# Kernel optimization log

Hardware: AMD Instinct MI355X
Metric: run time of the kernel (lower is better)

The kernel has to match this reference:

```python
import jax, jax.numpy as jnp
import numpy as np

B, S, D = 2, 2048, 1024
H, KVH, HD = 16, 1, 64
E, K, HID = 8, 2, 4096
EPS = 1e-5


def rmsnorm(x, scale):
    ms = jnp.mean(x * x, axis=-1, keepdims=True)
    return x * jax.lax.rsqrt(ms + EPS) * scale


def setup_inputs() -> dict:
    key = jax.random.key(0)
    ks = jax.random.split(key, 12)
    s = lambda k, shape, fan: jax.random.normal(k, shape, jnp.float32) * (fan ** -0.5)
    return {
        "x": jax.random.normal(ks[0], (B, S, D), jnp.float32),
        "g_pre_mqa": jnp.ones((D,), jnp.float32),
        "g_post_mqa": jnp.ones((D,), jnp.float32),
        "g_pre_moe": jnp.ones((D,), jnp.float32),
        "g_post_moe": jnp.ones((D,), jnp.float32),
        "Wq": s(ks[1], (D, H * HD), D),
        "Wk": s(ks[2], (D, KVH * HD), D),
        "Wv": s(ks[3], (D, KVH * HD), D),
        "Wo": s(ks[4], (H * HD, D), H * HD),
        "Wg": s(ks[5], (D, E), D),
        "We1": s(ks[6], (E, D, HID), D),
        "We2": s(ks[7], (E, HID, D), HID),
    }


def mqa(x, Wq, Wk, Wv, Wo):
    b, s, _ = x.shape
    q = (x @ Wq).reshape(b, s, H, HD).transpose(0, 2, 1, 3)     # [B,H,S,hd]
    k = (x @ Wk).reshape(b, s, KVH, HD).transpose(0, 2, 1, 3)   # [B,1,S,hd]
    v = (x @ Wv).reshape(b, s, KVH, HD).transpose(0, 2, 1, 3)
    scores = jnp.einsum('bhqd,bhkd->bhqk', q, jnp.broadcast_to(k, (b, H, s, HD))) / np.sqrt(HD)
    probs = jax.nn.softmax(scores, axis=-1)  # note: no causal mask, matching _standard_attention
    out = jnp.einsum('bhqk,bhkd->bhqd', probs, jnp.broadcast_to(v, (b, H, s, HD)))
    out = out.transpose(0, 2, 1, 3).reshape(b, s, H * HD)
    return out @ Wo


def moe(h, Wg, We1, We2):
    logits = h @ Wg                       # [B,S,E]
    probs = jax.nn.softmax(logits, axis=-1)
    topv, topi = jax.lax.top_k(probs, K)  # [B,S,K]
    # scatter top-k probs into full expert vector (non-chosen experts -> 0)
    routing = jnp.sum(jax.nn.one_hot(topi, E, dtype=h.dtype) * topv[..., None], axis=-2)  # [B,S,E]
    mid = jax.nn.gelu(jnp.einsum('bsd,edh->bseh', h, We1))
    eo = jnp.einsum('bseh,ehd->bsed', mid, We2)
    out = jnp.einsum('bse,bsed->bsd', routing, eo)
    return out, probs


def reference(x, g_pre_mqa, g_post_mqa, g_pre_moe, g_post_moe, Wq, Wk, Wv, Wo, Wg, We1, We2):
    # inference path: dropout and router noise disabled (training=False)
    x = x + rmsnorm(mqa(rmsnorm(x, g_pre_mqa), Wq, Wk, Wv, Wo), g_post_mqa)
    moe_out, routing_probs = moe(rmsnorm(x, g_pre_moe), Wg, We1, We2)
    x = x + rmsnorm(moe_out, g_post_moe)
    return x, routing_probs
```

## Files before the change

kernel.cpp:

```cpp
#include <hip/hip_runtime.h>
#include <hip/hip_bf16.h>
#include <math.h>

#define NTOK   4096
#define DMODEL 1024
#define SEQL   2048
#define QKVW   1152
#define NH     16
#define HDIM   64
#define NE     8
#define HIDD   4096
#define EPSV   1e-5f
#define KT     32

#define ASCL   256.f
#define WSCL   4096.f
#define OUTSCL (1.f/1048576.f)

typedef __attribute__((ext_vector_type(8))) short bf16x8;
typedef __attribute__((ext_vector_type(8))) _Float16 f16x8;
typedef __attribute__((ext_vector_type(4))) _Float16 f16x4;
typedef __attribute__((ext_vector_type(4))) float f32x4;

__device__ __forceinline__ short f2b(float x){
  __hip_bfloat16 h = __float2bfloat16(x);
  return *reinterpret_cast<short*>(&h);
}
__device__ __forceinline__ float b2f(short s){
  __hip_bfloat16 h = *reinterpret_cast<__hip_bfloat16*>(&s);
  return __bfloat162float(h);
}
__device__ __forceinline__ void split3(float x, short& a, short& b, short& c){
  a = f2b(x);
  float r1 = x - b2f(a);
  b = f2b(r1);
  float r2 = r1 - b2f(b);
  c = f2b(r2);
}
__device__ __forceinline__ void split2h(float x, _Float16& a, _Float16& b){
  a = (_Float16)x;
  b = (_Float16)(x - (float)a);
}

__global__ __launch_bounds__(256) void transpose_conv_kernel(
    const float* __restrict__ in, short* __restrict__ out,
    int R, int C, long inb, long outb)
{
  __shared__ float tile[32][33];
  in  += (size_t)blockIdx.z * inb;
  out += (size_t)blockIdx.z * outb;
  int c0 = blockIdx.x*32, r0 = blockIdx.y*32;
  int tx = threadIdx.x & 31, ty = threadIdx.x >> 5;
  #pragma unroll
  for (int i=0;i<4;i++)
    tile[ty+i*8][tx] = in[(size_t)(r0+ty+i*8)*C + c0+tx];
  __syncthreads();
  #pragma unroll
  for (int i=0;i<4;i++)
    out[(size_t)(c0+ty+i*8)*R + r0+tx] = f2b(tile[tx][ty+i*8]);
}

__global__ __launch_bounds__(256) void transpose_split2f16_kernel(
    const float* __restrict__ in, _Float16* __restrict__ o1, _Float16* __restrict__ o2,
    int R, int C, int rowOff, int outLD)
{
  __shared__ float tile[32][33];
  int c0 = blockIdx.x*32, r0 = blockIdx.y*32;
  int tx = threadIdx.x & 31, ty = threadIdx.x >> 5;
  #pragma unroll
  for (int i=0;i<4;i++)
    tile[ty+i*8][tx] = in[(size_t)(r0+ty+i*8)*C + c0+tx];
  __syncthreads();
  #pragma unroll
  for (int i=0;i<4;i++){
    float v = tile[tx][ty+i*8] * WSCL;
    _Float16 a,b; split2h(v,a,b);
    size_t idx = (size_t)(c0+ty+i*8+rowOff)*outLD + r0+tx;
    o1[idx]=a; o2[idx]=b;
  }
}

__global__ __launch_bounds__(256) void rms_split2_kernel(
    const float* __restrict__ x, const float* __restrict__ g,
    _Float16* __restrict__ o1, _Float16* __restrict__ o2)
{
  int row = blockIdx.x, tid = threadIdx.x;
  const float4* xr = (const float4*)(x + (size_t)row*DMODEL);
  float4 v = xr[tid];
  float ss = v.x*v.x + v.y*v.y + v.z*v.z + v.w*v.w;
  #pragma unroll
  for (int off=32; off; off>>=1) ss += __shfl_down(ss, off);
  __shared__ float red[4];
  if ((tid&63)==0) red[tid>>6] = ss;
  __syncthreads();
  float rs = rsqrtf((red[0]+red[1]+red[2]+red[3])*(1.f/1024.f) + EPSV) * ASCL;
  float4 gv = ((const float4*)g)[tid];
  float o[4] = {v.x*rs*gv.x, v.y*rs*gv.y, v.z*rs*gv.z, v.w*rs*gv.w};
  f16x4 s1,s2;
  #pragma unroll
  for (int c=0;c<4;c++){ _Float16 a,b; split2h(o[c],a,b); s1[c]=a; s2[c]=b; }
  size_t base = (size_t)row*DMODEL + tid*4;
  *(f16x4*)(o1+base) = s1; *(f16x4*)(o2+base) = s2;
}

__global__ void split3_flat_kernel(const float* __restrict__ in,
    short* __restrict__ o1, short* __restrict__ o2, short* __restrict__ o3, int n4)
{
  int i = blockIdx.x*256 + threadIdx.x;
  if (i >= n4) return;
  float4 v = ((const float4*)in)[i];
  short4 s1,s2,s3;
  split3(v.x, s1.x, s2.x, s3.x);
  split3(v.y, s1.y, s2.y, s3.y);
  split3(v.z, s1.z, s2.z, s3.z);
  split3(v.w, s1.w, s2.w, s3.w);
  ((short4*)o1)[i]=s1; ((short4*)o2)[i]=s2; ((short4*)o3)[i]=s3;
}

__global__ __launch_bounds__(256) void vtrans_split3_kernel(
    const float* __restrict__ qkv,
    short* __restrict__ o1, short* __restrict__ o2, short* __restrict__ o3)
{
  __shared__ float tile[32][33];
  int s0 = blockIdx.x*32, d0 = blockIdx.y*32, b = blockIdx.z;
  int tx = threadIdx.x & 31, ty = threadIdx.x >> 5;
  #pragma unroll
  for (int i=0;i<4;i++)
    tile[ty+i*8][tx] = qkv[(size_t)(b*SEQL + s0+ty+i*8)*QKVW + DMODEL+HDIM + d0+tx];
  __syncthreads();
  #pragma unroll
  for (int i=0;i<4;i++){
    float v = tile[tx][ty+i*8];
    short a,bs,c; split3(v,a,bs,c);
    size_t idx = (size_t)(b*HDIM + d0+ty+i*8)*SEQL + s0+tx;
    o1[idx]=a; o2[idx]=bs; o3[idx]=c;
  }
}

__global__ __launch_bounds__(256) void gemm_f16x2_kernel(
    const _Float16* __restrict__ a1, const _Float16* __restrict__ a2,
    const _Float16* __restrict__ b1, const _Float16* __restrict__ b2,
    float* __restrict__ C, int K, int ldc, float outscale)
{
  __shared__ _Float16 lsA[2][128*40];
  __shared__ _Float16 lsB[2][128*40];
  int m0 = blockIdx.y*128, n0 = blockIdx.x*128;
  int tid = threadIdx.x, wave = tid>>6, lane = tid&63;
  int g = lane>>4, li = lane&15;
  int wm = (wave>>1)*64, wn = (wave&1)*64;
  const _Float16* Ap[2] = {a1,a2};
  const _Float16* Bp[2] = {b1,b2};
  f32x4 acc[4][4] = {};
  for (int k0=0; k0<K; k0+=32){
    #pragma unroll
    for (int p=0;p<2;p++){
      #pragma unroll
      for (int i=0;i<2;i++){
        int c = tid + 256*i;
        int row = c>>2, col = (c&3)*8;
        *(f16x8*)&lsA[p][row*40+col] = *(const f16x8*)(Ap[p] + (size_t)(m0+row)*K + k0+col);
        *(f16x8*)&lsB[p][row*40+col] = *(const f16x8*)(Bp[p] + (size_t)(n0+row)*K + k0+col);
      }
    }
    __syncthreads();
    #pragma unroll
    for (int i=0;i<2;i++){
      f16x8 af[4];
      #pragma unroll
      for (int m=0;m<4;m++) af[m] = *(f16x8*)&lsA[i][(wm+m*16+li)*40 + g*8];
      #pragma unroll
      for (int j=0;j<2-i;j++){
        #pragma unroll
        for (int n=0;n<4;n++){
          f16x8 bfr = *(f16x8*)&lsB[j][(wn+n*16+li)*40 + g*8];
          #pragma unroll
          for (int m=0;m<4;m++)
            acc[m][n] = __builtin_amdgcn_mfma_f32_16x16x32_f16(af[m], bfr, acc[m][n], 0,0,0);
        }
      }
    }
    __syncthreads();
  }
  #pragma unroll
  for (int m=0;m<4;m++){
    int lr0 = wm + m*16 + g*4;
    #pragma unroll
    for (int n=0;n<4;n++){
      int col = n0 + wn + n*16 + li;
      #pragma unroll
      for (int r=0;r<4;r++)
        C[(size_t)(m0+lr0+r)*ldc + col] = acc[m][n][r]*outscale;
    }
  }
}

__global__ __launch_bounds__(256) void attn_bf16x3_kernel(
    const short* __restrict__ q1, const short* __restrict__ q2, const short* __restrict__ q3,
    const short* __restrict__ v1, const short* __restrict__ v2, const short* __restrict__ v3,
    _Float16* __restrict__ o1, _Float16* __restrict__ o2)
{
  __shared__ short Qs[128*200];
  __shared__ short Ks[32*200];
  __shared__ short Vs[64*104];
  int qt = blockIdx.x, h = blockIdx.y, b = blockIdx.z;
  int tid = threadIdx.x, wave = tid>>6, lane = tid&63;
  int g = lane>>4, li = lane&15;
  size_t qbase = (size_t)b*SEQL + qt*128;
  const short* qsrc[3] = {q1,q2,q3};
  const short* vsrc[3] = {v1,v2,v3};
  #pragma unroll
  for (int i=0;i<12;i++){
    int c = tid + 256*i;
    int row = c/24, sub = c - row*24;
    int p = sub>>3, d = (sub&7)*8;
    *(bf16x8*)&Qs[row*200 + p*64 + d] =
        *(const bf16x8*)(qsrc[p] + (qbase+row)*QKVW + h*HDIM + d);
  }
  float m_run[2] = {-1e30f,-1e30f}, l_run[2] = {0.f,0.f};
  f32x4 acc_o[4][2] = {};
  int src1 = (((2*g)&3)<<4) + li;
  int src2 = (((2*g+1)&3)<<4) + li;
  bool hi_half = (g>=2);

  for (int kvt=0; kvt<SEQL/KT; kvt++){
    __syncthreads();
    #pragma unroll
    for (int i=0;i<3;i++){
      int c = tid + 256*i;
      {
        int row = c/24, sub = c - row*24;
        int p = sub>>3, d = (sub&7)*8;
        *(bf16x8*)&Ks[row*200 + p*64 + d] =
          *(const bf16x8*)(qsrc[p] + ((size_t)b*SEQL + kvt*KT + row)*QKVW + DMODEL + d);
      }
      {
        int row = c/12, sub = c - row*12;
        int p = sub>>2, s8 = (sub&3)*8;
        *(bf16x8*)&Vs[row*104 + p*32 + s8] =
          *(const bf16x8*)(vsrc[p] + ((size_t)b*HDIM + row)*SEQL + kvt*KT + s8);
      }
    }
    __syncthreads();
    f32x4 s_acc[2][2] = {};
    #pragma unroll
    for (int i=0;i<3;i++){
      #pragma unroll
      for (int kk=0;kk<2;kk++){
        bf16x8 af[2];
        #pragma unroll
        for (int mf=0;mf<2;mf++)
          af[mf] = *(bf16x8*)&Ks[(mf*16+li)*200 + i*64 + kk*32 + g*8];
        #pragma unroll
        for (int j=0;j<3-i;j++){
          #pragma unroll
          for (int nf=0;nf<2;nf++){
            bf16x8 bfr = *(bf16x8*)&Qs[(wave*32+nf*16+li)*200 + j*64 + kk*32 + g*8];
            #pragma unroll
            for (int mf=0;mf<2;mf++)
              s_acc[mf][nf] = __builtin_amdgcn_mfma_f32_16x16x32_bf16(af[mf], bfr, s_acc[mf][nf], 0,0,0);
          }
        }
      }
    }
    float p[2][2][4];
    #pragma unroll
    for (int nf=0;nf<2;nf++){
      float mx = -1e30f;
      #pragma unroll
      for (int mf=0;mf<2;mf++)
        #pragma unroll
        for (int r=0;r<4;r++) mx = fmaxf(mx, s_acc[mf][nf][r]);
      mx = fmaxf(mx, __shfl_xor(mx,16));
      mx = fmaxf(mx, __shfl_xor(mx,32));
      mx *= 0.125f;
      if (!__all(mx <= m_run[nf] + 8.f)){
        float mn = fmaxf(m_run[nf], mx);
        float al = __expf(m_run[nf] - mn);
        m_run[nf] = mn;
        l_run[nf] *= al;
        #pragma unroll
        for (int mfd=0; mfd<4; mfd++){
          acc_o[mfd][nf][0]*=al; acc_o[mfd][nf][1]*=al;
          acc_o[mfd][nf][2]*=al; acc_o[mfd][nf][3]*=al;
        }
      }
      float rsum = 0.f;
      #pragma unroll
      for (int mf=0;mf<2;mf++)
        #pragma unroll
        for (int r=0;r<4;r++){
          float pv = __expf(s_acc[mf][nf][r]*0.125f - m_run[nf]);
          p[mf][nf][r] = pv; rsum += pv;
        }
      rsum += __shfl_xor(rsum,16);
      rsum += __shfl_xor(rsum,32);
      l_run[nf] += rsum;
    }
    bf16x8 fp_frag[2][3];
    #pragma unroll
    for (int nf=0;nf<2;nf++){
      float p8[8];
      #pragma unroll
      for (int jj=0;jj<4;jj++){
        float v0 = __shfl(p[0][nf][jj], src1);
        float vv1 = __shfl(p[1][nf][jj], src1);
        p8[jj] = hi_half ? vv1 : v0;
        float w0 = __shfl(p[0][nf][jj], src2);
        float w1 = __shfl(p[1][nf][jj], src2);
        p8[4+jj] = hi_half ? w1 : w0;
      }
      #pragma unroll
      for (int jj=0;jj<8;jj++){
        short xa,xb,xc; split3(p8[jj], xa,xb,xc);
        fp_frag[nf][0][jj]=xa; fp_frag[nf][1][jj]=xb; fp_frag[nf][2][jj]=xc;
      }
    }
    #pragma unroll
    for (int vj=0;vj<3;vj++){
      bf16x8 av[4];
      #pragma unroll
      for (int mfd=0;mfd<4;mfd++)
        av[mfd] = *(bf16x8*)&Vs[(mfd*16+li)*104 + vj*32 + g*8];
      #pragma unroll
      for (int pi=0; pi<3-vj; pi++)
        #pragma unroll
        for (int mfd=0;mfd<4;mfd++)
          #pragma unroll
          for (int nf=0;nf<2;nf++)
            acc_o[mfd][nf] = __builtin_amdgcn_mfma_f32_16x16x32_bf16(av[mfd], fp_frag[nf][pi], acc_o[mfd][nf], 0,0,0);
    }
  }
  #pragma unroll
  for (int nf=0;nf<2;nf++){
    float inv = ASCL/l_run[nf];
    size_t q = qbase + wave*32 + nf*16 + li;
    #pragma unroll
    for (int mfd=0;mfd<4;mfd++){
      int d0 = mfd*16 + g*4;
      f16x4 sa,sb;
      #pragma unroll
      for (int r=0;r<4;r++){
        _Float16 xa,xb; split2h(acc_o[mfd][nf][r]*inv, xa,xb);
        sa[r]=xa; sb[r]=xb;
      }
      size_t base = q*DMODEL + h*HDIM + d0;
      *(f16x4*)(o1+base)=sa; *(f16x4*)(o2+base)=sb;
    }
  }
}

__global__ __launch_bounds__(256) void attnres_kernel(
    const float* __restrict__ x, const float* __restrict__ ao,
    const float* __restrict__ gpost, const float* __restrict__ gpre,
    float* __restrict__ x2, short* __restrict__ h)
{
  int row = blockIdx.x, tid = threadIdx.x;
  float4 a  = ((const float4*)(ao + (size_t)row*DMODEL))[tid];
  float4 xv = ((const float4*)(x  + (size_t)row*DMODEL))[tid];
  float ss = a.x*a.x + a.y*a.y + a.z*a.z + a.w*a.w;
  #pragma unroll
  for (int off=32; off; off>>=1) ss += __shfl_down(ss, off);
  __shared__ float red[4];
  if ((tid&63)==0) red[tid>>6] = ss;
  __syncthreads();
  float rs1 = rsqrtf((red[0]+red[1]+red[2]+red[3])*(1.f/1024.f) + EPSV);
  float4 gp = ((const float4*)gpost)[tid];
  float4 o;
  o.x = xv.x + a.x*rs1*gp.x; o.y = xv.y + a.y*rs1*gp.y;
  o.z = xv.z + a.z*rs1*gp.z; o.w = xv.w + a.w*rs1*gp.w;
  ((float4*)(x2 + (size_t)row*DMODEL))[tid] = o;
  float s2 = o.x*o.x + o.y*o.y + o.z*o.z + o.w*o.w;
  __syncthreads();
  #pragma unroll
  for (int off=32; off; off>>=1) s2 += __shfl_down(s2, off);
  if ((tid&63)==0) red[tid>>6] = s2;
  __syncthreads();
  float rs2 = rsqrtf((red[0]+red[1]+red[2]+red[3])*(1.f/1024.f) + EPSV);
  float4 gm = ((const float4*)gpre)[tid];
  short4 hs;
  hs.x = f2b(o.x*rs2*gm.x); hs.y = f2b(o.y*rs2*gm.y);
  hs.z = f2b(o.z*rs2*gm.z); hs.w = f2b(o.w*rs2*gm.w);
  *(short4*)(h + (size_t)row*DMODEL + tid*4) = hs;
}

__global__ __launch_bounds__(64) void router_kernel(
    const float* __restrict__ x2, const float* __restrict__ g, const float* __restrict__ Wg,
    float* __restrict__ probs_out, int* __restrict__ tok_list, float* __restrict__ w_list,
    int* __restrict__ counts)
{
  int t = blockIdx.x, lane = threadIdx.x;
  const float4* xr = (const float4*)(x2 + (size_t)t*DMODEL);
  float4 v[4]; float ss = 0.f;
  #pragma unroll
  for (int i=0;i<4;i++){ v[i] = xr[lane + 64*i];
    ss += v[i].x*v[i].x + v[i].y*v[i].y + v[i].z*v[i].z + v[i].w*v[i].w; }
  #pragma unroll
  for (int off=32; off; off>>=1) ss += __shfl_xor(ss, off);
  float rs = rsqrtf(ss*(1.f/1024.f) + EPSV);
  float le[8] = {0,0,0,0,0,0,0,0};
  #pragma unroll
  for (int i=0;i<4;i++){
    int jb = (lane + 64*i)*4;
    float hv[4] = {v[i].x, v[i].y, v[i].z, v[i].w};
    #pragma unroll
    for (int c=0;c<4;c++){
      float hj = hv[c]*rs*g[jb+c];
      const float* wrow = Wg + (size_t)(jb+c)*NE;
      #pragma unroll
      for (int ee=0;ee<8;ee++) le[ee] += hj*wrow[ee];
    }
  }
  #pragma unroll
  for (int ee=0;ee<8;ee++)
    #pragma unroll
    for (int off=32; off; off>>=1) le[ee] += __shfl_xor(le[ee], off);
  float mx = le[0];
  #pragma unroll
  for (int ee=1;ee<8;ee++) mx = fmaxf(mx, le[ee]);
  float p[8], s = 0.f;
  #pragma unroll
  for (int ee=0;ee<8;ee++){ p[ee] = expf(le[ee]-mx); s += p[ee]; }
  float inv = 1.f/s;
  #pragma unroll
  for (int ee=0;ee<8;ee++) p[ee] *= inv;
  if (lane < 8) probs_out[(size_t)t*NE + lane] = p[lane];
  if (lane == 0){
    int i1 = 0;
    #pragma unroll
    for (int ee=1;ee<8;ee++) if (p[ee] > p[i1]) i1 = ee;
    int i2 = (i1==0) ? 1 : 0;
    #pragma unroll
    for (int ee=0;ee<8;ee++) if (ee != i1 && p[ee] > p[i2]) i2 = ee;
    int pos = atomicAdd(&counts[i1], 1);
    tok_list[i1*NTOK+pos] = t;
    w_list[i1*NTOK+pos] = p[i1];
    pos = atomicAdd(&counts[i2], 1);
    tok_list[i2*NTOK+pos] = t | (1<<16);
    w_list[i2*NTOK+pos] = p[i2];
  }
}

__global__ void prefix_kernel(const int* __restrict__ counts, int* __restrict__ bases){
  if (threadIdx.x == 0){
    int a = 0;
    for (int ee=0;ee<8;ee++){ bases[ee] = a; a += counts[ee]; }
  }
}

__global__ __launch_bounds__(256) void moe_gemm1_kernel(
    const short* __restrict__ h, const short* __restrict__ we1t,
    const int* __restrict__ tok_list, const int* __restrict__ counts,
    const int* __restrict__ bases, short* __restrict__ mid)
{
  int e = blockIdx.z;
  int cnt = counts[e];
  int m0 = blockIdx.y*128, n0 = blockIdx.x*128;
  if (m0 >= cnt) return;
  int base = bases[e];
  const short* Bt = we1t + (size_t)e*HIDD*DMODEL;
  const int* tl = tok_list + e*NTOK;
  __shared__ short lsA[128*40];
  __shared__ short lsB[128*40];
  int tid = threadIdx.x, wave = tid>>6, lane = tid&63;
  int wm = (wave>>1)*64, wn = (wave&1)*64;
  const short* aptr[2]; const short* bptr[2];
  #pragma unroll
  for (int i=0;i<2;i++){
    int c = tid + 256*i; int row = c>>2;
    int rr = min(m0+row, cnt-1);
    aptr[i] = h + (size_t)(tl[rr] & 0xFFFF)*DMODEL;
    bptr[i] = Bt + (size_t)(n0+row)*DMODEL;
  }
  f32x4 acc[4][4] = {};
  for (int k0=0; k0<DMODEL; k0+=32){
    #pragma unroll
    for (int i=0;i<2;i++){
      int c = tid + 256*i; int row = c>>2, col = (c&3)*8;
      *(bf16x8*)&lsA[row*40+col] = *(const bf16x8*)(aptr[i]+k0+col);
      *(bf16x8*)&lsB[row*40+col] = *(const bf16x8*)(bptr[i]+k0+col);
    }
    __syncthreads();
    bf16x8 af[4], bfr[4];
    #pragma unroll
    for (int m=0;m<4;m++) af[m] = *(bf16x8*)&lsA[(wm+m*16+(lane&15))*40 + (lane>>4)*8];
    #pragma unroll
    for (int n=0;n<4;n++) bfr[n] = *(bf16x8*)&lsB[(wn+n*16+(lane&15))*40 + (lane>>4)*8];
    #pragma unroll
    for (int m=0;m<4;m++)
      #pragma unroll
      for (int n=0;n<4;n++)
        acc[m][n] = __builtin_amdgcn_mfma_f32_16x16x32_bf16(af[m], bfr[n], acc[m][n], 0,0,0);
    __syncthreads();
  }
  #pragma unroll
  for (int m=0;m<4;m++){
    int lr0 = wm + m*16 + ((lane>>4)<<2);
    #pragma unroll
    for (int n=0;n<4;n++){
      int col = n0 + wn + n*16 + (lane&15);
      #pragma unroll
      for (int r=0;r<4;r++){
        int gr = m0 + lr0 + r;
        if (gr < cnt){
          float tval = acc[m][n][r];
          float u = 1.5957691216057308f*(tval + 0.044715f*tval*tval*tval);
          float ge = tval / (1.f + __expf(-u));
          mid[(size_t)(base+gr)*HIDD + col] = f2b(ge);
        }
      }
    }
  }
}

__global__ __launch_bounds__(256) void moe_gemm2_kernel(
    const short* __restrict__ mid, const short* __restrict__ we2t,
    const int* __restrict__ tok_list, const float* __restrict__ w_list,
    const int* __restrict__ counts, const int* __restrict__ bases,
    float* __restrict__ eo)
{
  int e = blockIdx.z;
  int cnt = counts[e];
  int m0 = blockIdx.y*128, n0 = blockIdx.x*128;
  if (m0 >= cnt) return;
  int base = bases[e];
  const short* A  = mid + (size_t)base*HIDD;
  const short* Bt = we2t + (size_t)e*DMODEL*HIDD;
  const int* tl = tok_list + e*NTOK;
  const float* wl = w_list + e*NTOK;
  __shared__ short lsA[128*40];
  __shared__ short lsB[128*40];
  int tid = threadIdx.x, wave = tid>>6, lane = tid&63;
  int wm = (wave>>1)*64, wn = (wave&1)*64;
  const short* aptr[2]; const short* bptr[2];
  #pragma unroll
  for (int i=0;i<2;i++){
    int c = tid + 256*i; int row = c>>2;
    int rr = min(m0+row, cnt-1);
    aptr[i] = A + (size_t)rr*HIDD;
    bptr[i] = Bt + (size_t)(n0+row)*HIDD;
  }
  f32x4 acc[4][4] = {};
  for (int k0=0; k0<HIDD; k0+=32){
    #pragma unroll
    for (int i=0;i<2;i++){
      int c = tid + 256*i; int row = c>>2, col = (c&3)*8;
      *(bf16x8*)&lsA[row*40+col] = *(const bf16x8*)(aptr[i]+k0+col);
      *(bf16x8*)&lsB[row*40+col] = *(const bf16x8*)(bptr[i]+k0+col);
    }
    __syncthreads();
    bf16x8 af[4], bfr[4];
    #pragma unroll
    for (int m=0;m<4;m++) af[m] = *(bf16x8*)&lsA[(wm+m*16+(lane&15))*40 + (lane>>4)*8];
    #pragma unroll
    for (int n=0;n<4;n++) bfr[n] = *(bf16x8*)&lsB[(wn+n*16+(lane&15))*40 + (lane>>4)*8];
    #pragma unroll
    for (int m=0;m<4;m++)
      #pragma unroll
      for (int n=0;n<4;n++)
        acc[m][n] = __builtin_amdgcn_mfma_f32_16x16x32_bf16(af[m], bfr[n], acc[m][n], 0,0,0);
    __syncthreads();
  }
  #pragma unroll
  for (int m=0;m<4;m++){
    int lr0 = wm + m*16 + ((lane>>4)<<2);
    #pragma unroll
    for (int n=0;n<4;n++){
      int col = n0 + wn + n*16 + (lane&15);
      #pragma unroll
      for (int r=0;r<4;r++){
        int gr = m0 + lr0 + r;
        if (gr < cnt){
          int pv = tl[gr];
          eo[((size_t)(pv>>16)*NTOK + (pv & 0xFFFF))*DMODEL + col] = wl[gr]*acc[m][n][r];
        }
      }
    }
  }
}

__global__ __launch_bounds__(256) void final_kernel(
    const float* __restrict__ x2, const float* __restrict__ eo,
    const float* __restrict__ g, float* __restrict__ out)
{
  int row = blockIdx.x, tid = threadIdx.x;
  float4 m0 = ((const float4*)(eo + (size_t)row*DMODEL))[tid];
  float4 m1 = ((const float4*)(eo + (size_t)(NTOK+row)*DMODEL))[tid];
  float4 mv;
  mv.x = m0.x+m1.x; mv.y = m0.y+m1.y; mv.z = m0.z+m1.z; mv.w = m0.w+m1.w;
  float4 xv = ((const float4*)(x2  + (size_t)row*DMODEL))[tid];
  float ss = mv.x*mv.x + mv.y*mv.y + mv.z*mv.z + mv.w*mv.w;
  #pragma unroll
  for (int off=32; off; off>>=1) ss += __shfl_down(ss, off);
  __shared__ float red[4];
  if ((tid&63)==0) red[tid>>6] = ss;
  __syncthreads();
  float rs = rsqrtf((red[0]+red[1]+red[2]+red[3])*(1.f/1024.f) + EPSV);
  float4 gv = ((const float4*)g)[tid];
  float4 o;
  o.x = xv.x + mv.x*rs*gv.x; o.y = xv.y + mv.y*rs*gv.y;
  o.z = xv.z + mv.z*rs*gv.z; o.w = xv.w + mv.w*rs*gv.w;
  ((float4*)(out + (size_t)row*DMODEL))[tid] = o;
}

extern "C" void kernel_launch(void* const* d_in, const int* in_sizes, int n_in,
                              void* d_out, int out_size, void* d_ws, size_t ws_size,
                              hipStream_t stream) {
  (void)in_sizes; (void)n_in; (void)out_size; (void)ws_size;
  const float* x          = (const float*)d_in[0];
  const float* g_pre_mqa  = (const float*)d_in[1];
  const float* g_post_mqa = (const float*)d_in[2];
  const float* g_pre_moe  = (const float*)d_in[3];
  const float* g_post_moe = (const float*)d_in[4];
  const float* Wq         = (const float*)d_in[5];
  const float* Wk         = (const float*)d_in[6];
  const float* Wv         = (const float*)d_in[7];
  const float* Wo         = (const float*)d_in[8];
  const float* Wg         = (const float*)d_in[9];
  const float* We1        = (const float*)d_in[10];
  const float* We2        = (const float*)d_in[11];

  float* out_x = (float*)d_out;
  float* out_probs = out_x + (size_t)NTOK*DMODEL;

  char* p = (char*)d_ws;
  size_t off = 0;
  auto alloc = [&](size_t bytes)->char*{
    char* r = p + off; off = (off + bytes + 255) & ~(size_t)255; return r; };

  short* we1t = (short*)alloc((size_t)NE*HIDD*DMODEL*2);
  short* we2t = (short*)alloc((size_t)NE*DMODEL*HIDD*2);
  short* mid  = (short*)alloc((size_t)2*NTOK*HIDD*2);

  char* regA = alloc((size_t)2*NTOK*DMODEL*2);
  _Float16* xn1p1 = (_Float16*)regA;
  _Float16* xn1p2 = (_Float16*)(regA + (size_t)NTOK*DMODEL*2);
  float* ao       = (float*)regA;

  _Float16* wqkvT1 = (_Float16*)alloc((size_t)QKVW*DMODEL*2);
  _Float16* wqkvT2 = (_Float16*)alloc((size_t)QKVW*DMODEL*2);
  _Float16* woT1   = (_Float16*)alloc((size_t)DMODEL*DMODEL*2);
  _Float16* woT2   = (_Float16*)alloc((size_t)DMODEL*DMODEL*2);

  char* regB = alloc((size_t)NTOK*QKVW*4);
  float* qkv = (float*)regB;
  _Float16* attnp1 = (_Float16*)regB;
  _Float16* attnp2 = (_Float16*)(regB + (size_t)NTOK*DMODEL*2);

  char* regC = alloc((size_t)2*NTOK*DMODEL*4 + (size_t)NTOK*DMODEL*2);
  short* qkvs1 = (short*)regC;
  short* qkvs2 = (short*)(regC + (size_t)NTOK*QKVW*2);
  short* qkvs3 = (short*)(regC + (size_t)2*NTOK*QKVW*2);
  float* eo    = (float*)regC;
  short* hbuf  = (short*)(regC + (size_t)2*NTOK*DMODEL*4);

  short* vt1 = (short*)alloc((size_t)2*HDIM*SEQL*2);
  short* vt2 = (short*)alloc((size_t)2*HDIM*SEQL*2);
  short* vt3 = (short*)alloc((size_t)2*HDIM*SEQL*2);
  float* x2  = (float*)alloc((size_t)NTOK*DMODEL*4);
  int*   tok_l  = (int*)  alloc((size_t)NE*NTOK*4);
  float* w_l    = (float*)alloc((size_t)NE*NTOK*4);
  int*   counts = (int*)  alloc(256);
  int*   bases  = (int*)  alloc(256);

  transpose_conv_kernel<<<dim3(HIDD/32, DMODEL/32, NE), 256, 0, stream>>>(
      We1, we1t, DMODEL, HIDD, (long)DMODEL*HIDD, (long)HIDD*DMODEL);
  transpose_conv_kernel<<<dim3(DMODEL/32, HIDD/32, NE), 256, 0, stream>>>(
      We2, we2t, HIDD, DMODEL, (long)HIDD*DMODEL, (long)DMODEL*HIDD);
  transpose_split2f16_kernel<<<dim3(DMODEL/32, DMODEL/32), 256, 0, stream>>>(
      Wq, wqkvT1, wqkvT2, DMODEL, DMODEL, 0, DMODEL);
  transpose_split2f16_kernel<<<dim3(HDIM/32, DMODEL/32), 256, 0, stream>>>(
      Wk, wqkvT1, wqkvT2, DMODEL, HDIM, DMODEL, DMODEL);
  transpose_split2f16_kernel<<<dim3(HDIM/32, DMODEL/32), 256, 0, stream>>>(
      Wv, wqkvT1, wqkvT2, DMODEL, HDIM, DMODEL+HDIM, DMODEL);
  transpose_split2f16_kernel<<<dim3(DMODEL/32, DMODEL/32), 256, 0, stream>>>(
      Wo, woT1, woT2, DMODEL, DMODEL, 0, DMODEL);

  rms_split2_kernel<<<NTOK, 256, 0, stream>>>(x, g_pre_mqa, xn1p1, xn1p2);
  gemm_f16x2_kernel<<<dim3(QKVW/128, NTOK/128), 256, 0, stream>>>(
      xn1p1, xn1p2, wqkvT1, wqkvT2, qkv, DMODEL, QKVW, OUTSCL);
  split3_flat_kernel<<<(NTOK*QKVW/4 + 255)/256, 256, 0, stream>>>(
      qkv, qkvs1, qkvs2, qkvs3, NTOK*QKVW/4);
  vtrans_split3_kernel<<<dim3(SEQL/32, HDIM/32, 2), 256, 0, stream>>>(qkv, vt1, vt2, vt3);
  attn_bf16x3_kernel<<<dim3(SEQL/128, NH, 2), 256, 0, stream>>>(
      qkvs1, qkvs2, qkvs3, vt1, vt2, vt3, attnp1, attnp2);
  gemm_f16x2_kernel<<<dim3(DMODEL/128, NTOK/128), 256, 0, stream>>>(
      attnp1, attnp2, woT1, woT2, ao, DMODEL, DMODEL, OUTSCL);
  attnres_kernel<<<NTOK, 256, 0, stream>>>(x, ao, g_post_mqa, g_pre_moe, x2, hbuf);

  hipMemsetAsync(counts, 0, 32, stream);
  router_kernel<<<NTOK, 64, 0, stream>>>(x2, g_pre_moe, Wg, out_probs, tok_l, w_l, counts);
  prefix_kernel<<<1, 64, 0, stream>>>(counts, bases);
  moe_gemm1_kernel<<<dim3(HIDD/128, NTOK/128, NE), 256, 0, stream>>>(
      hbuf, we1t, tok_l, counts, bases, mid);
  moe_gemm2_kernel<<<dim3(DMODEL/128, NTOK/128, NE), 256, 0, stream>>>(
      mid, we2t, tok_l, w_l, counts, bases, eo);
  final_kernel<<<NTOK, 256, 0, stream>>>(x2, eo, g_post_moe, out_x);
}
```

Before: 894.3 us.

## Use direct global-to-LDS loads in GEMMs and keep attention Q in registers

Replaces the register-staged global→LDS copies in the f16x2 GEMM and both MoE GEMMs with `__builtin_amdgcn_global_load_lds` 16-byte transfers. LDS rows become unpadded (stride 32) to fit the contiguous per-wave layout these loads write. The attention kernel drops its large Q shared buffer and holds each wave's Q fragments in registers instead. This cuts VGPR round-trips and LDS traffic and frees LDS for occupancy, at the cost of possible LDS bank conflicts from the removed padding and higher register pressure in attention.

```diff
diff --git a/kernel.cpp b/kernel.cpp
--- a/kernel.cpp
+++ b/kernel.cpp
@@ -22,6 +22,12 @@
 typedef __attribute__((ext_vector_type(4))) _Float16 f16x4;
 typedef __attribute__((ext_vector_type(4))) float f32x4;
 
+#define GLOBAL_AS __attribute__((address_space(1)))
+#define LDS_AS    __attribute__((address_space(3)))
+__device__ __forceinline__ void gl_lds16(const void* g, void* l){
+  __builtin_amdgcn_global_load_lds((const GLOBAL_AS void*)g, (LDS_AS void*)l, 16u, 0, 0u);
+}
+
 __device__ __forceinline__ short f2b(float x){
   __hip_bfloat16 h = __float2bfloat16(x);
   return *reinterpret_cast<short*>(&h);
@@ -142,37 +148,43 @@
     const _Float16* __restrict__ b1, const _Float16* __restrict__ b2,
     float* __restrict__ C, int K, int ldc, float outscale)
 {
-  __shared__ _Float16 lsA[2][128*40];
-  __shared__ _Float16 lsB[2][128*40];
+  __shared__ _Float16 lsA[2][128*32];
+  __shared__ _Float16 lsB[2][128*32];
   int m0 = blockIdx.y*128, n0 = blockIdx.x*128;
   int tid = threadIdx.x, wave = tid>>6, lane = tid&63;
   int g = lane>>4, li = lane&15;
   int wm = (wave>>1)*64, wn = (wave&1)*64;
   const _Float16* Ap[2] = {a1,a2};
   const _Float16* Bp[2] = {b1,b2};
+  int srow = wave*32 + (lane>>2), scol = (lane&3)*8;
+  const _Float16* gA[2][2]; const _Float16* gB[2][2];
+  #pragma unroll
+  for (int p=0;p<2;p++)
+    #pragma unroll
+    for (int i=0;i<2;i++){
+      gA[p][i] = Ap[p] + (size_t)(m0+srow+i*16)*K + scol;
+      gB[p][i] = Bp[p] + (size_t)(n0+srow+i*16)*K + scol;
+    }
   f32x4 acc[4][4] = {};
   for (int k0=0; k0<K; k0+=32){
     #pragma unroll
-    for (int p=0;p<2;p++){
+    for (int p=0;p<2;p++)
       #pragma unroll
       for (int i=0;i<2;i++){
-        int c = tid + 256*i;
-        int row = c>>2, col = (c&3)*8;
-        *(f16x8*)&lsA[p][row*40+col] = *(const f16x8*)(Ap[p] + (size_t)(m0+row)*K + k0+col);
-        *(f16x8*)&lsB[p][row*40+col] = *(const f16x8*)(Bp[p] + (size_t)(n0+row)*K + k0+col);
-      }
-    }
+        gl_lds16(gA[p][i]+k0, &lsA[p][(wave*32+i*16)*32]);
+        gl_lds16(gB[p][i]+k0, &lsB[p][(wave*32+i*16)*32]);
+      }
     __syncthreads();
     #pragma unroll
     for (int i=0;i<2;i++){
       f16x8 af[4];
       #pragma unroll
-      for (int m=0;m<4;m++) af[m] = *(f16x8*)&lsA[i][(wm+m*16+li)*40 + g*8];
+      for (int m=0;m<4;m++) af[m] = *(f16x8*)&lsA[i][(wm+m*16+li)*32 + g*8];
       #pragma unroll
       for (int j=0;j<2-i;j++){
         #pragma unroll
         for (int n=0;n<4;n++){
-          f16x8 bfr = *(f16x8*)&lsB[j][(wn+n*16+li)*40 + g*8];
+          f16x8 bfr = *(f16x8*)&lsB[j][(wn+n*16+li)*32 + g*8];
           #pragma unroll
           for (int m=0;m<4;m++)
             acc[m][n] = __builtin_amdgcn_mfma_f32_16x16x32_f16(af[m], bfr, acc[m][n], 0,0,0);
@@ -199,7 +211,6 @@
     const short* __restrict__ v1, const short* __restrict__ v2, const short* __restrict__ v3,
     _Float16* __restrict__ o1, _Float16* __restrict__ o2)
 {
-  __shared__ short Qs[128*200];
   __shared__ short Ks[32*200];
   __shared__ short Vs[64*104];
   int qt = blockIdx.x, h = blockIdx.y, b = blockIdx.z;
@@ -208,13 +219,15 @@
   size_t qbase = (size_t)b*SEQL + qt*128;
   const short* qsrc[3] = {q1,q2,q3};
   const short* vsrc[3] = {v1,v2,v3};
-  #pragma unroll
-  for (int i=0;i<12;i++){
-    int c = tid + 256*i;
-    int row = c/24, sub = c - row*24;
-    int p = sub>>3, d = (sub&7)*8;
-    *(bf16x8*)&Qs[row*200 + p*64 + d] =
-        *(const bf16x8*)(qsrc[p] + (qbase+row)*QKVW + h*HDIM + d);
+  bf16x8 qf[2][3][2];
+  #pragma unroll
+  for (int nf=0;nf<2;nf++){
+    size_t qrow = qbase + wave*32 + nf*16 + li;
+    #pragma unroll
+    for (int j=0;j<3;j++)
+      #pragma unroll
+      for (int kk=0;kk<2;kk++)
+        qf[nf][j][kk] = *(const bf16x8*)(qsrc[j] + qrow*QKVW + h*HDIM + kk*32 + g*8);
   }
   float m_run[2] = {-1e30f,-1e30f}, l_run[2] = {0.f,0.f};
   f32x4 acc_o[4][2] = {};
@@ -254,10 +267,9 @@
         for (int j=0;j<3-i;j++){
           #pragma unroll
           for (int nf=0;nf<2;nf++){
-            bf16x8 bfr = *(bf16x8*)&Qs[(wave*32+nf*16+li)*200 + j*64 + kk*32 + g*8];
             #pragma unroll
             for (int mf=0;mf<2;mf++)
-              s_acc[mf][nf] = __builtin_amdgcn_mfma_f32_16x16x32_bf16(af[mf], bfr, s_acc[mf][nf], 0,0,0);
+              s_acc[mf][nf] = __builtin_amdgcn_mfma_f32_16x16x32_bf16(af[mf], qf[nf][j][kk], s_acc[mf][nf], 0,0,0);
           }
         }
       }
@@ -459,32 +471,32 @@
   int base = bases[e];
   const short* Bt = we1t + (size_t)e*HIDD*DMODEL;
   const int* tl = tok_list + e*NTOK;
-  __shared__ short lsA[128*40];
-  __shared__ short lsB[128*40];
+  __shared__ short lsA[128*32];
+  __shared__ short lsB[128*32];
   int tid = threadIdx.x, wave = tid>>6, lane = tid&63;
+  int li = lane&15, g = lane>>4;
   int wm = (wave>>1)*64, wn = (wave&1)*64;
-  const short* aptr[2]; const short* bptr[2];
+  int srow = wave*32 + (lane>>2), scol = (lane&3)*8;
+  const short* gA[2]; const short* gB[2];
   #pragma unroll
   for (int i=0;i<2;i++){
-    int c = tid + 256*i; int row = c>>2;
-    int rr = min(m0+row, cnt-1);
-    aptr[i] = h + (size_t)(tl[rr] & 0xFFFF)*DMODEL;
-    bptr[i] = Bt + (size_t)(n0+row)*DMODEL;
+    int rr = min(m0+srow+i*16, cnt-1);
+    gA[i] = h + (size_t)(tl[rr] & 0xFFFF)*DMODEL + scol;
+    gB[i] = Bt + (size_t)(n0+srow+i*16)*DMODEL + scol;
   }
   f32x4 acc[4][4] = {};
   for (int k0=0; k0<DMODEL; k0+=32){
     #pragma unroll
     for (int i=0;i<2;i++){
-      int c = tid + 256*i; int row = c>>2, col = (c&3)*8;
-      *(bf16x8*)&lsA[row*40+col] = *(const bf16x8*)(aptr[i]+k0+col);
-      *(bf16x8*)&lsB[row*40+col] = *(const bf16x8*)(bptr[i]+k0+col);
+      gl_lds16(gA[i]+k0, &lsA[(wave*32+i*16)*32]);
+      gl_lds16(gB[i]+k0, &lsB[(wave*32+i*16)*32]);
     }
     __syncthreads();
     bf16x8 af[4], bfr[4];
     #pragma unroll
-    for (int m=0;m<4;m++) af[m] = *(bf16x8*)&lsA[(wm+m*16+(lane&15))*40 + (lane>>4)*8];
-    #pragma unroll
-    for (int n=0;n<4;n++) bfr[n] = *(bf16x8*)&lsB[(wn+n*16+(lane&15))*40 + (lane>>4)*8];
+    for (int m=0;m<4;m++) af[m] = *(bf16x8*)&lsA[(wm+m*16+li)*32 + g*8];
+    #pragma unroll
+    for (int n=0;n<4;n++) bfr[n] = *(bf16x8*)&lsB[(wn+n*16+li)*32 + g*8];
     #pragma unroll
     for (int m=0;m<4;m++)
       #pragma unroll
@@ -494,10 +506,10 @@
   }
   #pragma unroll
   for (int m=0;m<4;m++){
-    int lr0 = wm + m*16 + ((lane>>4)<<2);
+    int lr0 = wm + m*16 + (g<<2);
     #pragma unroll
     for (int n=0;n<4;n++){
-      int col = n0 + wn + n*16 + (lane&15);
+      int col = n0 + wn + n*16 + li;
       #pragma unroll
       for (int r=0;r<4;r++){
         int gr = m0 + lr0 + r;
@@ -527,32 +539,32 @@
   const short* Bt = we2t + (size_t)e*DMODEL*HIDD;
   const int* tl = tok_list + e*NTOK;
   const float* wl = w_list + e*NTOK;
-  __shared__ short lsA[128*40];
-  __shared__ short lsB[128*40];
+  __shared__ short lsA[128*32];
+  __shared__ short lsB[128*32];
   int tid = threadIdx.x, wave = tid>>6, lane = tid&63;
+  int li = lane&15, g = lane>>4;
   int wm = (wave>>1)*64, wn = (wave&1)*64;
-  const short* aptr[2]; const short* bptr[2];
+  int srow = wave*32 + (lane>>2), scol = (lane&3)*8;
+  const short* gA[2]; const short* gB[2];
   #pragma unroll
   for (int i=0;i<2;i++){
-    int c = tid + 256*i; int row = c>>2;
-    int rr = min(m0+row, cnt-1);
-    aptr[i] = A + (size_t)rr*HIDD;
-    bptr[i] = Bt + (size_t)(n0+row)*HIDD;
+    int rr = min(m0+srow+i*16, cnt-1);
+    gA[i] = A + (size_t)rr*HIDD + scol;
+    gB[i] = Bt + (size_t)(n0+srow+i*16)*HIDD + scol;
   }
   f32x4 acc[4][4] = {};
   for (int k0=0; k0<HIDD; k0+=32){
     #pragma unroll
     for (int i=0;i<2;i++){
-      int c = tid + 256*i; int row = c>>2, col = (c&3)*8;
-      *(bf16x8*)&lsA[row*40+col] = *(const bf16x8*)(aptr[i]+k0+col);
-      *(bf16x8*)&lsB[row*40+col] = *(const bf16x8*)(bptr[i]+k0+col);
+      gl_lds16(gA[i]+k0, &lsA[(wave*32+i*16)*32]);
+      gl_lds16(gB[i]+k0, &lsB[(wave*32+i*16)*32]);
     }
     __syncthreads();
     bf16x8 af[4], bfr[4];
     #pragma unroll
-    for (int m=0;m<4;m++) af[m] = *(bf16x8*)&lsA[(wm+m*16+(lane&15))*40 + (lane>>4)*8];
-    #pragma unroll
-    for (int n=0;n<4;n++) bfr[n] = *(bf16x8*)&lsB[(wn+n*16+(lane&15))*40 + (lane>>4)*8];
+    for (int m=0;m<4;m++) af[m] = *(bf16x8*)&lsA[(wm+m*16+li)*32 + g*8];
+    #pragma unroll
+    for (int n=0;n<4;n++) bfr[n] = *(bf16x8*)&lsB[(wn+n*16+li)*32 + g*8];
     #pragma unroll
     for (int m=0;m<4;m++)
       #pragma unroll
@@ -562,10 +574,10 @@
   }
   #pragma unroll
   for (int m=0;m<4;m++){
-    int lr0 = wm + m*16 + ((lane>>4)<<2);
+    int lr0 = wm + m*16 + (g<<2);
     #pragma unroll
     for (int n=0;n<4;n++){
-      int col = n0 + wn + n*16 + (lane&15);
+      int col = n0 + wn + n*16 + li;
       #pragma unroll
       for (int r=0;r<4;r++){
         int gr = m0 + lr0 + r;
```

After: 839.8 us. -6.1%, faster.
